# Kernel optimization log

Measured on AMD Instinct MI355X. Metric: run time of the kernel, lower is better.

Reference implementation:

```python
import jax, jax.numpy as jnp
import numpy as np

B = 524288   # batch
I = 12       # input_props
R = 6        # output_props (rules)
J = 2        # templates per rule
L = 2        # feature width
V = 4        # variables


def setup_inputs() -> dict:
    key = jax.random.key(0)
    ks = jax.random.split(key, 7)
    concrete_features = jax.random.uniform(ks[0], (B, I, L), dtype=jnp.float32)
    templates = jax.random.uniform(ks[1], (R, J, L), dtype=jnp.float32)           # U(0,1)
    gammas = jax.random.uniform(ks[2], (R, J, L), dtype=jnp.float32) * 0.4 + 0.4  # U(0.4,0.8)
    body_W = jax.random.normal(ks[3], (R, J, V, L), dtype=jnp.float32) * 0.5
    body_b = jax.random.normal(ks[4], (R, J, V), dtype=jnp.float32) * 0.1
    head_W = jax.random.normal(ks[5], (R, L, V), dtype=jnp.float32) * 0.5
    head_b = jax.random.normal(ks[6], (R, L), dtype=jnp.float32) * 0.1
    return {"concrete_features": concrete_features, "templates": templates,
            "gammas": gammas, "body_W": body_W, "body_b": body_b,
            "head_W": head_W, "head_b": head_b}


def reference(concrete_features, templates, gammas, body_W, body_b, head_W, head_b):
    # "sigmoid" in the original is clamp(x, 0, 1)
    g = jnp.clip(gammas, 0.0, 1.0)            # [R,J,L]
    w = 1.0 - g                               # per-dim match weight
    # match_scores[b,r,j,i] = sum_l w[r,j,l] * (templates[r,j,l] - f[b,i,l])^2
    # expand the square to avoid materializing a [B,R,J,I,L] tensor
    c0 = jnp.sum(w * templates * templates, axis=-1)                       # [R,J]
    cross = jnp.einsum('rjl,bil->brji', w * templates, concrete_features)  # [B,R,J,I]
    quad = jnp.einsum('rjl,bil->brji', w, concrete_features ** 2)          # [B,R,J,I]
    match_scores = c0[None, :, :, None] - 2.0 * cross + quad               # [B,R,J,I]
    attn = jax.nn.softmax(-match_scores, axis=-1)                          # over input_props
    # soft-selected feature per (rule, template): [B,R,J,L]
    selected = jnp.einsum('brji,bil->brjl', attn, concrete_features)
    # body Linear per (r,j), then sum over j (biases also sum over j)
    captured = jnp.einsum('brjl,rjvl->brv', selected, body_W) + jnp.sum(body_b, axis=1)  # [B,R,V]
    # head Linear per rule
    out = jnp.einsum('brv,rlv->brl', captured, head_W) + head_b            # [B,R,L]
    return out
```

## Files before the change

### kernel.cpp

```cpp
#include <hip/hip_runtime.h>

#define NI 12
#define NR 6
#define NJ 2
#define NL 2
#define NV 4

typedef float v2f __attribute__((ext_vector_type(2)));


__global__ __launch_bounds__(256) void
abstraction_fused(const float* __restrict__ feat,
                  const float* __restrict__ templates,
                  const float* __restrict__ gammas,
                  const float* __restrict__ body_W,
                  const float* __restrict__ body_b,
                  const float* __restrict__ head_W,
                  const float* __restrict__ head_b,
                  float* __restrict__ out, int B) {
    __shared__ float sG[NR * NJ * 5];
    __shared__ float sM[NR * NL * NJ * NL];
    __shared__ float sC[NR * NL];

    const int t = threadIdx.x;
    const float LOG2E = 1.4426950408889634f;

    if (t < NR * NJ) {
        const int g = t;
        float g0 = fminf(fmaxf(gammas[g * NL + 0], 0.f), 1.f);
        float g1 = fminf(fmaxf(gammas[g * NL + 1], 0.f), 1.f);
        float w0 = 1.f - g0, w1 = 1.f - g1;
        float t0 = templates[g * NL + 0], t1 = templates[g * NL + 1];
        float wt0 = w0 * t0, wt1 = w1 * t1;
        float c0 = wt0 * t0 + wt1 * t1;
        sG[g * 5 + 0] = 2.f * LOG2E * wt0;
        sG[g * 5 + 1] = 2.f * LOG2E * wt1;
        sG[g * 5 + 2] = -LOG2E * w0;
        sG[g * 5 + 3] = -LOG2E * w1;
        sG[g * 5 + 4] = -LOG2E * c0;
    } else if (t >= 64 && t < 64 + NR * NL) {
        const int idx = t - 64;
        const int r = idx >> 1, l = idx & 1;
        float acc = head_b[r * NL + l];
        #pragma unroll
        for (int v = 0; v < NV; ++v) {
            float bs = body_b[(r * NJ + 0) * NV + v] + body_b[(r * NJ + 1) * NV + v];
            acc = fmaf(head_W[(r * NL + l) * NV + v], bs, acc);
        }
        sC[idx] = acc;
    } else if (t >= 128 && t < 128 + NR * NL * NJ * NL) {
        const int idx = t - 128;
        const int lp = idx & 1, j = (idx >> 1) & 1, l = (idx >> 2) & 1, r = idx >> 3;
        float acc = 0.f;
        #pragma unroll
        for (int v = 0; v < NV; ++v)
            acc = fmaf(head_W[(r * NL + l) * NV + v],
                       body_W[((r * NJ + j) * NV + v) * NL + lp], acc);
        sM[idx] = acc;
    }
    __syncthreads();

    const int b = blockIdx.x * blockDim.x + t;
    if (b >= B) return;

    const float4* fp = (const float4*)(feat + (size_t)b * (NI * NL));
    float f0[NI], f1[NI];
    #pragma unroll
    for (int k = 0; k < 6; ++k) {
        float4 v = fp[k];
        f0[2 * k + 0] = v.x; f1[2 * k + 0] = v.y;
        f0[2 * k + 1] = v.z; f1[2 * k + 1] = v.w;
    }

    float o[NR * NL];
    #pragma unroll
    for (int r = 0; r < NR; ++r) {
        float o0 = sC[r * 2 + 0];
        float o1 = sC[r * 2 + 1];
        #pragma unroll
        for (int j = 0; j < NJ; ++j) {
            const int g = r * NJ + j;
            const v2f A0 = sG[g * 5 + 0];
            const v2f A1 = sG[g * 5 + 1];
            const v2f W0 = sG[g * 5 + 2];
            const v2f W1 = sG[g * 5 + 3];
            const v2f Cn = sG[g * 5 + 4];
            v2f den = 0.f, a0 = 0.f, a1 = 0.f;
            #pragma unroll
            for (int i = 0; i < NI; i += 2) {
                v2f X0 = { f0[i], f0[i + 1] };
                v2f X1 = { f1[i], f1[i + 1] };
                v2f n = __builtin_elementwise_fma(X0, __builtin_elementwise_fma(W0, X0, A0), Cn);
                n = __builtin_elementwise_fma(X1, __builtin_elementwise_fma(W1, X1, A1), n);
                v2f p = { __builtin_amdgcn_exp2f(n.x), __builtin_amdgcn_exp2f(n.y) };
                den += p;
                a0 = __builtin_elementwise_fma(p, X0, a0);
                a1 = __builtin_elementwise_fma(p, X1, a1);
            }
            float d = den.x + den.y;
            float rinv = __builtin_amdgcn_rcpf(d);
            float s0 = (a0.x + a0.y) * rinv;
            float s1 = (a1.x + a1.y) * rinv;
            const float m00 = sM[((r * 2 + 0) * 2 + j) * 2 + 0];
            const float m01 = sM[((r * 2 + 0) * 2 + j) * 2 + 1];
            const float m10 = sM[((r * 2 + 1) * 2 + j) * 2 + 0];
            const float m11 = sM[((r * 2 + 1) * 2 + j) * 2 + 1];
            o0 = fmaf(s0, m00, o0); o0 = fmaf(s1, m01, o0);
            o1 = fmaf(s0, m10, o1); o1 = fmaf(s1, m11, o1);
        }
        o[r * 2 + 0] = o0;
        o[r * 2 + 1] = o1;
    }

    float4* op = (float4*)(out + (size_t)b * (NR * NL));
    op[0] = make_float4(o[0], o[1], o[2], o[3]);
    op[1] = make_float4(o[4], o[5], o[6], o[7]);
    op[2] = make_float4(o[8], o[9], o[10], o[11]);
}

extern "C" void kernel_launch(void* const* d_in, const int* in_sizes, int n_in,
                              void* d_out, int out_size, void* d_ws, size_t ws_size,
                              hipStream_t stream) {
    (void)n_in; (void)out_size; (void)d_ws; (void)ws_size;
    const float* feat      = (const float*)d_in[0];
    const float* templates = (const float*)d_in[1];
    const float* gammas    = (const float*)d_in[2];
    const float* body_W    = (const float*)d_in[3];
    const float* body_b    = (const float*)d_in[4];
    const float* head_W    = (const float*)d_in[5];
    const float* head_b    = (const float*)d_in[6];
    float* out = (float*)d_out;

    int B = in_sizes[0] / (NI * NL);
    int blocks = (B + 255) / 256;
    hipLaunchKernelGGL(abstraction_fused, dim3(blocks), dim3(256), 0, stream,
                       feat, templates, gammas, body_W, body_b, head_W, head_b,
                       out, B);
}
```

Measured before the change: 109.5 us.

## Stage feature loads via global_load_lds and coalesce output through LDS

Features are now loaded with coalesced global_load_lds (direct global-to-LDS) per wave, overlapping with the parameter precompute before the barrier. Outputs are staged back through LDS so the global stores are fully coalesced. The block size drops to 128 and the final mixing is vectorised with packed v2f FMAs. This targets strided per-thread 96-byte loads and 48-byte stores, at the cost of extra LDS traffic and a larger LDS footprint per block.

```diff
diff --git a/kernel.cpp b/kernel.cpp
--- a/kernel.cpp
+++ b/kernel.cpp
@@ -6,24 +6,44 @@
 #define NL 2
 #define NV 4
 
+#define BLK 128
+#define EPB BLK
+
 typedef float v2f __attribute__((ext_vector_type(2)));
 
-
-__global__ __launch_bounds__(256) void
-abstraction_fused(const float* __restrict__ feat,
+__global__ __launch_bounds__(BLK) void
+abstraction_fused(const float4* __restrict__ feat4,
                   const float* __restrict__ templates,
                   const float* __restrict__ gammas,
                   const float* __restrict__ body_W,
                   const float* __restrict__ body_b,
                   const float* __restrict__ head_W,
                   const float* __restrict__ head_b,
-                  float* __restrict__ out, int B) {
-    __shared__ float sG[NR * NJ * 5];
-    __shared__ float sM[NR * NL * NJ * NL];
-    __shared__ float sC[NR * NL];
+                  float4* __restrict__ out4, int B) {
+    __shared__ __align__(16) float4 sF[BLK * 6];
+    __shared__ __align__(16) float sG[NR * NJ * 5];
+    __shared__ __align__(16) float sMt[NR * NJ * NL * NL];
+    __shared__ __align__(16) float sC[NR * NL];
 
     const int t = threadIdx.x;
+    const int lane = t & 63;
+    const int w = t >> 6;
     const float LOG2E = 1.4426950408889634f;
+
+    const int blockElem0 = blockIdx.x * EPB;
+    const bool fullTile = (blockElem0 + EPB) <= B;
+
+    if (fullTile) {
+        const int base4 = (blockElem0 + w * 64) * 6;
+        const float4* gp = feat4 + base4 + lane;
+        #pragma unroll
+        for (int k = 0; k < 6; ++k) {
+            __builtin_amdgcn_global_load_lds(
+                (const __attribute__((address_space(1))) void*)(gp + k * 64),
+                (__attribute__((address_space(3))) void*)&sF[w * 384 + k * 64],
+                16, 0, 0);
+        }
+    }
 
     if (t < NR * NJ) {
         const int g = t;
@@ -38,8 +58,8 @@
         sG[g * 5 + 2] = -LOG2E * w0;
         sG[g * 5 + 3] = -LOG2E * w1;
         sG[g * 5 + 4] = -LOG2E * c0;
-    } else if (t >= 64 && t < 64 + NR * NL) {
-        const int idx = t - 64;
+    } else if (t >= 16 && t < 16 + NR * NL) {
+        const int idx = t - 16;
         const int r = idx >> 1, l = idx & 1;
         float acc = head_b[r * NL + l];
         #pragma unroll
@@ -48,35 +68,42 @@
             acc = fmaf(head_W[(r * NL + l) * NV + v], bs, acc);
         }
         sC[idx] = acc;
-    } else if (t >= 128 && t < 128 + NR * NL * NJ * NL) {
-        const int idx = t - 128;
-        const int lp = idx & 1, j = (idx >> 1) & 1, l = (idx >> 2) & 1, r = idx >> 3;
+    } else if (t >= 32 && t < 32 + NR * NJ * NL * NL) {
+        const int idx = t - 32;
+        const int l = idx & 1, lp = (idx >> 1) & 1, j = (idx >> 2) & 1, r = idx >> 3;
         float acc = 0.f;
         #pragma unroll
         for (int v = 0; v < NV; ++v)
             acc = fmaf(head_W[(r * NL + l) * NV + v],
                        body_W[((r * NJ + j) * NV + v) * NL + lp], acc);
-        sM[idx] = acc;
+        sMt[idx] = acc;
     }
+
     __syncthreads();
 
-    const int b = blockIdx.x * blockDim.x + t;
-    if (b >= B) return;
-
-    const float4* fp = (const float4*)(feat + (size_t)b * (NI * NL));
     float f0[NI], f1[NI];
-    #pragma unroll
-    for (int k = 0; k < 6; ++k) {
-        float4 v = fp[k];
-        f0[2 * k + 0] = v.x; f1[2 * k + 0] = v.y;
-        f0[2 * k + 1] = v.z; f1[2 * k + 1] = v.w;
+    if (fullTile) {
+        #pragma unroll
+        for (int k = 0; k < 6; ++k) {
+            float4 v = sF[w * 384 + lane * 6 + k];
+            f0[2 * k + 0] = v.x; f1[2 * k + 0] = v.y;
+            f0[2 * k + 1] = v.z; f1[2 * k + 1] = v.w;
+        }
+    } else {
+        int e = blockElem0 + t; if (e >= B) e = B - 1;
+        const float4* fp = feat4 + (size_t)e * 6;
+        #pragma unroll
+        for (int k = 0; k < 6; ++k) {
+            float4 v = fp[k];
+            f0[2 * k + 0] = v.x; f1[2 * k + 0] = v.y;
+            f0[2 * k + 1] = v.z; f1[2 * k + 1] = v.w;
+        }
     }
 
     float o[NR * NL];
     #pragma unroll
     for (int r = 0; r < NR; ++r) {
-        float o0 = sC[r * 2 + 0];
-        float o1 = sC[r * 2 + 1];
+        v2f O = *(const v2f*)&sC[r * 2];
         #pragma unroll
         for (int j = 0; j < NJ; ++j) {
             const int g = r * NJ + j;
@@ -90,50 +117,64 @@
             for (int i = 0; i < NI; i += 2) {
                 v2f X0 = { f0[i], f0[i + 1] };
                 v2f X1 = { f1[i], f1[i + 1] };
-                v2f n = __builtin_elementwise_fma(X0, __builtin_elementwise_fma(W0, X0, A0), Cn);
-                n = __builtin_elementwise_fma(X1, __builtin_elementwise_fma(W1, X1, A1), n);
+                v2f n = __builtin_elementwise_fma(
+                            X0, __builtin_elementwise_fma(W0, X0, A0),
+                            __builtin_elementwise_fma(
+                                X1, __builtin_elementwise_fma(W1, X1, A1), Cn));
                 v2f p = { __builtin_amdgcn_exp2f(n.x), __builtin_amdgcn_exp2f(n.y) };
                 den += p;
                 a0 = __builtin_elementwise_fma(p, X0, a0);
                 a1 = __builtin_elementwise_fma(p, X1, a1);
             }
+            const v2f M0 = *(const v2f*)&sMt[(g * 2 + 0) * 2];
+            const v2f M1 = *(const v2f*)&sMt[(g * 2 + 1) * 2];
             float d = den.x + den.y;
             float rinv = __builtin_amdgcn_rcpf(d);
-            float s0 = (a0.x + a0.y) * rinv;
-            float s1 = (a1.x + a1.y) * rinv;
-            const float m00 = sM[((r * 2 + 0) * 2 + j) * 2 + 0];
-            const float m01 = sM[((r * 2 + 0) * 2 + j) * 2 + 1];
-            const float m10 = sM[((r * 2 + 1) * 2 + j) * 2 + 0];
-            const float m11 = sM[((r * 2 + 1) * 2 + j) * 2 + 1];
-            o0 = fmaf(s0, m00, o0); o0 = fmaf(s1, m01, o0);
-            o1 = fmaf(s0, m10, o1); o1 = fmaf(s1, m11, o1);
+            v2f s0 = (a0.x + a0.y) * rinv;
+            v2f s1 = (a1.x + a1.y) * rinv;
+            O = __builtin_elementwise_fma(s0, M0,
+                __builtin_elementwise_fma(s1, M1, O));
         }
-        o[r * 2 + 0] = o0;
-        o[r * 2 + 1] = o1;
+        o[r * 2 + 0] = O.x;
+        o[r * 2 + 1] = O.y;
     }
 
-    float4* op = (float4*)(out + (size_t)b * (NR * NL));
-    op[0] = make_float4(o[0], o[1], o[2], o[3]);
-    op[1] = make_float4(o[4], o[5], o[6], o[7]);
-    op[2] = make_float4(o[8], o[9], o[10], o[11]);
+    if (fullTile) {
+        #pragma unroll
+        for (int c = 0; c < 3; ++c)
+            sF[w * 384 + lane * 3 + c] =
+                make_float4(o[4 * c + 0], o[4 * c + 1], o[4 * c + 2], o[4 * c + 3]);
+        const int outBase4 = (blockElem0 + w * 64) * 3;
+        #pragma unroll
+        for (int c = 0; c < 3; ++c)
+            out4[outBase4 + c * 64 + lane] = sF[w * 384 + c * 64 + lane];
+    } else {
+        int e = blockElem0 + t;
+        if (e < B) {
+            float4* p = &out4[(size_t)e * 3];
+            p[0] = make_float4(o[0], o[1], o[2], o[3]);
+            p[1] = make_float4(o[4], o[5], o[6], o[7]);
+            p[2] = make_float4(o[8], o[9], o[10], o[11]);
+        }
+    }
 }
 
 extern "C" void kernel_launch(void* const* d_in, const int* in_sizes, int n_in,
                               void* d_out, int out_size, void* d_ws, size_t ws_size,
                               hipStream_t stream) {
     (void)n_in; (void)out_size; (void)d_ws; (void)ws_size;
-    const float* feat      = (const float*)d_in[0];
+    const float4* feat4    = (const float4*)d_in[0];
     const float* templates = (const float*)d_in[1];
     const float* gammas    = (const float*)d_in[2];
     const float* body_W    = (const float*)d_in[3];
     const float* body_b    = (const float*)d_in[4];
     const float* head_W    = (const float*)d_in[5];
     const float* head_b    = (const float*)d_in[6];
-    float* out = (float*)d_out;
+    float4* out4 = (float4*)d_out;
 
     int B = in_sizes[0] / (NI * NL);
-    int blocks = (B + 255) / 256;
-    hipLaunchKernelGGL(abstraction_fused, dim3(blocks), dim3(256), 0, stream,
-                       feat, templates, gammas, body_W, body_b, head_W, head_b,
-                       out, B);
+    int blocks = (B + EPB - 1) / EPB;
+    hipLaunchKernelGGL(abstraction_fused, dim3(blocks), dim3(BLK), 0, stream,
+                       feat4, templates, gammas, body_W, body_b, head_W, head_b,
+                       out4, B);
 }
```

After: 110.7 us. No clear change (+1.1%).
